# Performance work log

Measured on AMD Instinct MI355X. Metric: run time of the kernel, lower is better.

## Reference

```python
import jax, jax.numpy as jnp
import numpy as np

TEMPERATURE = 0.5  # module buffer `temperature`


def setup_inputs() -> dict:
    key = jax.random.key(0)
    emb_in = jax.random.normal(key, (8192, 1024), dtype=jnp.float32)
    return {"emb_in": emb_in}


def reference(emb_in):
    B = emb_in.shape[0]
    n = B // 4  # loop bound in the original module
    # F.normalize(emb_in, dim=1); after normalization cosine_similarity == dot product
    z = emb_in / jnp.linalg.norm(emb_in, axis=1, keepdims=True)
    S = jnp.matmul(z, z.T) / jnp.float32(TEMPERATURE)  # [B, B] sim / temperature
    rows = S[:n]  # only rows i < n are ever used               # [n, B]
    idx = jnp.arange(n)
    exp_rows = jnp.exp(rows)
    # denominator_i = sum_{k != i} exp(sim[i,k]/T) over the FULL batch dimension
    denom = exp_rows.sum(axis=1) - exp_rows[idx, idx]           # [n]
    log_denom = jnp.log(denom)
    # loss_ij = -(S[i,j] - log(denom_i)); summed over i < j < n.
    # For each i there are (n-1-i) values of j, each contributing log_denom[i].
    counts = (n - 1) - idx                                      # [n]
    sum_sim = jnp.sum(jnp.triu(rows[:, :n], k=1))               # sum_{i<j} S[i,j]/T
    loss = jnp.sum(counts.astype(log_denom.dtype) * log_denom) - sum_sim
    return (-2.0 / n) * (n - 1) * loss
```

## Files before the change

### kernel.cpp

```cpp
#include <hip/hip_runtime.h>
#include <stdint.h>


#define BDIM 1024
#define BROWS 8192
#define NROWS 2048

#define BM 128
#define BN 256
#define BKB 128
#define NKT (BDIM / BKB)

typedef __attribute__((ext_vector_type(4))) int i32x4;
typedef __attribute__((ext_vector_type(8))) int i32x8;
typedef __attribute__((ext_vector_type(4))) float f32x4;

static __device__ __forceinline__ unsigned char f2e4m3(float x) {
  uint32_t u = __float_as_uint(x);
  uint32_t s = (u >> 24) & 0x80u;
  uint32_t a = u & 0x7fffffffu;
  if (a == 0) return (unsigned char)s;
  int e = (int)(a >> 23) - 127;
  uint32_t m = a & 0x7fffffu;
  if (e >= -6) {
    uint32_t keep = m >> 20;
    uint32_t rest = m & 0xfffffu;
    keep += (rest > 0x80000u) || (rest == 0x80000u && (keep & 1u));
    uint32_t v = ((uint32_t)(e + 7) << 3) + keep;
    return (unsigned char)(s | v);
  }
  if (e < -10) return (unsigned char)s;
  uint32_t full = 0x800000u | m;
  int sh = 14 - e;
  uint32_t keep = full >> sh;
  uint32_t rest = full & ((1u << sh) - 1u);
  uint32_t half = 1u << (sh - 1);
  keep += (rest > half) || (rest == half && (keep & 1u));
  return (unsigned char)(s | keep);
}

static __device__ __forceinline__ void gload_lds16(const unsigned char* g, unsigned char* l) {
  __builtin_amdgcn_global_load_lds(
      (const __attribute__((address_space(1))) uint32_t*)(const void*)g,
      (__attribute__((address_space(3))) uint32_t*)(void*)l,
      16, 0, 0);
}

static __device__ __forceinline__ uint32_t pk4(float4 v, float inv) {
  return (uint32_t)f2e4m3(v.x * inv) | ((uint32_t)f2e4m3(v.y * inv) << 8) |
         ((uint32_t)f2e4m3(v.z * inv) << 16) | ((uint32_t)f2e4m3(v.w * inv) << 24);
}

__global__ __launch_bounds__(256) void normalize_kernel(const float* __restrict__ emb,
                                                        unsigned char* __restrict__ zb,
                                                        float* __restrict__ denom,
                                                        float* __restrict__ sumsim) {
  const int w = threadIdx.x >> 6;
  const int lane = threadIdx.x & 63;
  const int row = blockIdx.x * 4 + w;
  const float4* src = reinterpret_cast<const float4*>(emb + (size_t)row * BDIM);
  float4 v[4];
  float ss = 0.f;
#pragma unroll
  for (int i = 0; i < 4; i++) {
    v[i] = src[lane * 4 + i];
    ss += v[i].x * v[i].x + v[i].y * v[i].y + v[i].z * v[i].z + v[i].w * v[i].w;
  }
#pragma unroll
  for (int m = 1; m < 64; m <<= 1) ss += __shfl_xor(ss, m);
  const float inv = rsqrtf(ss);
  uint4 o;
  o.x = pk4(v[0], inv);
  o.y = pk4(v[1], inv);
  o.z = pk4(v[2], inv);
  o.w = pk4(v[3], inv);
  const int cp = (lane & 56) | ((lane & 7) ^ (row & 7));
  *reinterpret_cast<uint4*>(zb + (size_t)row * BDIM + cp * 16) = o;
  if (blockIdx.x < NROWS / 4 && lane == 0) denom[row] = 0.f;
  if (blockIdx.x == 0 && threadIdx.x == 0) sumsim[0] = 0.f;
}


__global__ __launch_bounds__(512, 4) void gemm_fused(const unsigned char* __restrict__ zb,
                                                     float* __restrict__ denom,
                                                     float* __restrict__ sumsim) {
  __shared__ unsigned char As[BM * BKB];
  __shared__ unsigned char Bs[BN * BKB];

  const int bx = blockIdx.x;
  const int xcd = bx & 7;
  const int idx = bx >> 3;
  const int jb = xcd * 4 + (idx & 3);
  const int ib = idx >> 2;
  const int i0 = ib * BM;
  const int j0 = jb * BN;

  const int t = threadIdx.x;
  const int lane = t & 63;
  const int w = t >> 6;
  const int WR = w >> 2;
  const int WC = w & 3;

  const int rsh = lane >> 3;
  const int lin = (lane & 7) * 16;

  const int q2 = lane >> 4;
  const int rsub = lane & 15;
  const int rk = rsub & 7;

  f32x4 acc[4][4] = {};

#define STG_A(g, kk) \
  gload_lds16(zb + (size_t)(i0 + (g) * 8 + rsh) * BDIM + (kk) + lin, &As[(g) * 8 * BKB])
#define STG_B(g, kk) \
  gload_lds16(zb + (size_t)(j0 + (g) * 8 + rsh) * BDIM + (kk) + lin, &Bs[(g) * 8 * BKB])

#define RD_FRAG(dst, base, row)                                                                                  \
  {                                                                                                              \
    const i32x4 lo = *reinterpret_cast<const i32x4*>(&base[(size_t)(row) * BKB + (((2 * q2) ^ rk) * 16)]);       \
    const i32x4 hi = *reinterpret_cast<const i32x4*>(&base[(size_t)(row) * BKB + (((2 * q2 + 1) ^ rk) * 16)]);   \
    dst[0] = lo[0]; dst[1] = lo[1]; dst[2] = lo[2]; dst[3] = lo[3];                                              \
    dst[4] = hi[0]; dst[5] = hi[1]; dst[6] = hi[2]; dst[7] = hi[3];                                              \
  }

#pragma unroll 1
  for (int kt = 0; kt < NKT; ++kt) {
    const int kk = kt * BKB;
    STG_A(2 * w, kk); STG_A(2 * w + 1, kk);
    STG_B(4 * w, kk); STG_B(4 * w + 1, kk);
    STG_B(4 * w + 2, kk); STG_B(4 * w + 3, kk);
    __syncthreads();

    i32x8 bb[4];
#pragma unroll
    for (int nn = 0; nn < 4; nn++) {
      RD_FRAG(bb[nn], Bs, WC * 64 + nn * 16 + rsub);
    }
    __builtin_amdgcn_s_setprio(1);
#pragma unroll
    for (int mm = 0; mm < 4; mm++) {
      i32x8 aa;
      RD_FRAG(aa, As, WR * 64 + mm * 16 + rsub);
#pragma unroll
      for (int nn = 0; nn < 4; nn++) {
        acc[mm][nn] = __builtin_amdgcn_mfma_scale_f32_16x16x128_f8f6f4(
            aa, bb[nn], acc[mm][nn], 0, 0, 0, 0x7f7f7f7f, 0, 0x7f7f7f7f);
      }
    }
    __builtin_amdgcn_s_setprio(0);
    __syncthreads();
  }

  const int hi4 = lane >> 4;
  const int col_l = lane & 15;
  float ssim = 0.f;
#pragma unroll
  for (int m = 0; m < 4; m++) {
    const int gibase = i0 + WR * 64 + m * 16 + hi4 * 4;
#pragma unroll
    for (int r = 0; r < 4; r++) {
      const int gi = gibase + r;
      float dsum = 0.f;
#pragma unroll
      for (int n = 0; n < 4; n++) {
        const int gj = j0 + WC * 64 + n * 16 + col_l;
        const float s = acc[m][n][r] * 2.0f;
        const float e = __expf(s);
        if (gj != gi) dsum += e;
        if (gj < NROWS && gi < gj) ssim += s;
      }
      dsum += __shfl_xor(dsum, 1);
      dsum += __shfl_xor(dsum, 2);
      dsum += __shfl_xor(dsum, 4);
      dsum += __shfl_xor(dsum, 8);
      if (col_l == 0) atomicAdd(&denom[gi], dsum);
    }
  }
#pragma unroll
  for (int msk = 1; msk < 64; msk <<= 1) ssim += __shfl_xor(ssim, msk);
  if (lane == 0 && j0 < NROWS) atomicAdd(sumsim, ssim);
}

__global__ __launch_bounds__(1024) void finalize(const float* __restrict__ denom,
                                                 const float* __restrict__ sumsim,
                                                 float* __restrict__ out) {
  const int t = threadIdx.x;
  double s = 0.0;
#pragma unroll
  for (int i = t; i < NROWS; i += 1024) {
    s += (double)(NROWS - 1 - i) * log((double)denom[i]);
  }
#pragma unroll
  for (int m = 1; m < 64; m <<= 1) s += __shfl_xor(s, m);
  __shared__ double ws_[16];
  if ((t & 63) == 0) ws_[t >> 6] = s;
  __syncthreads();
  if (t == 0) {
    double tot = 0.0;
#pragma unroll
    for (int i = 0; i < 16; i++) tot += ws_[i];
    const double loss = tot - (double)sumsim[0];
    out[0] = (float)(-2.0 / (double)NROWS * (double)(NROWS - 1) * loss);
  }
}

extern "C" void kernel_launch(void* const* d_in, const int* in_sizes, int n_in,
                              void* d_out, int out_size, void* d_ws, size_t ws_size,
                              hipStream_t stream) {
  const float* emb = (const float*)d_in[0];
  unsigned char* zb = (unsigned char*)d_ws;
  float* denom = (float*)((char*)d_ws + (size_t)BROWS * BDIM);
  float* sumsim = denom + NROWS;
  float* out = (float*)d_out;

  normalize_kernel<<<BROWS / 4, 256, 0, stream>>>(emb, zb, denom, sumsim);
  gemm_fused<<<(NROWS / BM) * (BROWS / BN), 512, 0, stream>>>(zb, denom, sumsim);
  finalize<<<1, 1024, 0, stream>>>(denom, sumsim, out);
}
```

Baseline: 59.02 us.

## Prefetch next K tile into registers while computing current tile

Replaces direct global-to-LDS loads with register-staged loads. The next K tile is issued before the MFMA loop and written to LDS after a barrier, so global latency overlaps with compute. This adds six uint4 registers per thread, which puts pressure on the 4-waves occupancy bound, and adds an extra barrier per iteration because LDS is still single-buffered.

```diff
diff --git a/kernel.cpp b/kernel.cpp
--- a/kernel.cpp
+++ b/kernel.cpp
@@ -39,13 +39,6 @@
   return (unsigned char)(s | keep);
 }
 
-static __device__ __forceinline__ void gload_lds16(const unsigned char* g, unsigned char* l) {
-  __builtin_amdgcn_global_load_lds(
-      (const __attribute__((address_space(1))) uint32_t*)(const void*)g,
-      (__attribute__((address_space(3))) uint32_t*)(void*)l,
-      16, 0, 0);
-}
-
 static __device__ __forceinline__ uint32_t pk4(float4 v, float inv) {
   return (uint32_t)f2e4m3(v.x * inv) | ((uint32_t)f2e4m3(v.y * inv) << 8) |
          ((uint32_t)f2e4m3(v.z * inv) << 16) | ((uint32_t)f2e4m3(v.w * inv) << 24);
@@ -103,17 +96,37 @@
 
   const int rsh = lane >> 3;
   const int lin = (lane & 7) * 16;
+  const unsigned char* gA0 = zb + (size_t)(i0 + (2 * w) * 8 + rsh) * BDIM + lin;
+  const unsigned char* gA1 = zb + (size_t)(i0 + (2 * w + 1) * 8 + rsh) * BDIM + lin;
+  const unsigned char* gB0 = zb + (size_t)(j0 + (4 * w) * 8 + rsh) * BDIM + lin;
+  const unsigned char* gB1 = zb + (size_t)(j0 + (4 * w + 1) * 8 + rsh) * BDIM + lin;
+  const unsigned char* gB2 = zb + (size_t)(j0 + (4 * w + 2) * 8 + rsh) * BDIM + lin;
+  const unsigned char* gB3 = zb + (size_t)(j0 + (4 * w + 3) * 8 + rsh) * BDIM + lin;
+  uint4* lA0 = reinterpret_cast<uint4*>(&As[((2 * w) * 8 + rsh) * BKB + lin]);
+  uint4* lA1 = reinterpret_cast<uint4*>(&As[((2 * w + 1) * 8 + rsh) * BKB + lin]);
+  uint4* lB0 = reinterpret_cast<uint4*>(&Bs[((4 * w) * 8 + rsh) * BKB + lin]);
+  uint4* lB1 = reinterpret_cast<uint4*>(&Bs[((4 * w + 1) * 8 + rsh) * BKB + lin]);
+  uint4* lB2 = reinterpret_cast<uint4*>(&Bs[((4 * w + 2) * 8 + rsh) * BKB + lin]);
+  uint4* lB3 = reinterpret_cast<uint4*>(&Bs[((4 * w + 3) * 8 + rsh) * BKB + lin]);
 
   const int q2 = lane >> 4;
   const int rsub = lane & 15;
   const int rk = rsub & 7;
 
   f32x4 acc[4][4] = {};
-
-#define STG_A(g, kk) \
-  gload_lds16(zb + (size_t)(i0 + (g) * 8 + rsh) * BDIM + (kk) + lin, &As[(g) * 8 * BKB])
-#define STG_B(g, kk) \
-  gload_lds16(zb + (size_t)(j0 + (g) * 8 + rsh) * BDIM + (kk) + lin, &Bs[(g) * 8 * BKB])
+  uint4 pA0, pA1, pB0, pB1, pB2, pB3;
+
+#define LOADP(kk)                                                       \
+  {                                                                     \
+    pA0 = *reinterpret_cast<const uint4*>(gA0 + (kk));                  \
+    pA1 = *reinterpret_cast<const uint4*>(gA1 + (kk));                  \
+    pB0 = *reinterpret_cast<const uint4*>(gB0 + (kk));                  \
+    pB1 = *reinterpret_cast<const uint4*>(gB1 + (kk));                  \
+    pB2 = *reinterpret_cast<const uint4*>(gB2 + (kk));                  \
+    pB3 = *reinterpret_cast<const uint4*>(gB3 + (kk));                  \
+  }
+#define WRITEP()                                                        \
+  { *lA0 = pA0; *lA1 = pA1; *lB0 = pB0; *lB1 = pB1; *lB2 = pB2; *lB3 = pB3; }
 
 #define RD_FRAG(dst, base, row)                                                                                  \
   {                                                                                                              \
@@ -123,13 +136,13 @@
     dst[4] = hi[0]; dst[5] = hi[1]; dst[6] = hi[2]; dst[7] = hi[3];                                              \
   }
 
+  LOADP(0);
+  WRITEP();
+  __syncthreads();
+
 #pragma unroll 1
   for (int kt = 0; kt < NKT; ++kt) {
-    const int kk = kt * BKB;
-    STG_A(2 * w, kk); STG_A(2 * w + 1, kk);
-    STG_B(4 * w, kk); STG_B(4 * w + 1, kk);
-    STG_B(4 * w + 2, kk); STG_B(4 * w + 3, kk);
-    __syncthreads();
+    if (kt + 1 < NKT) LOADP((kt + 1) * BKB);
 
     i32x8 bb[4];
 #pragma unroll
@@ -148,7 +161,12 @@
       }
     }
     __builtin_amdgcn_s_setprio(0);
+
     __syncthreads();
+    if (kt + 1 < NKT) {
+      WRITEP();
+      __syncthreads();
+    }
   }
 
   const int hi4 = lane >> 4;
```

Result: slower. 177.3 us (+200.5%).

## Pre-tile FP8 embeddings into MFMA fragment-order units for contiguous loads

Applied to the files above, without the earlier changes.

The normalize kernel now writes the FP8 matrix in 16-row by 128-byte units, with bytes already arranged so each lane's MFMA fragment sits at lane*16 and lane*16+1024. The GEMM stages each unit with two fully contiguous 1KB global-to-LDS loads and reads fragments with plain linear LDS accesses, dropping the XOR swizzle arithmetic. The intent is better coalescing of global loads and conflict-free LDS reads. It ties the workspace layout to the tile shape.

```diff
diff --git a/kernel.cpp b/kernel.cpp
--- a/kernel.cpp
+++ b/kernel.cpp
@@ -8,8 +8,7 @@
 
 #define BM 128
 #define BN 256
-#define BKB 128
-#define NKT (BDIM / BKB)
+#define NKT 8
 
 typedef __attribute__((ext_vector_type(4))) int i32x4;
 typedef __attribute__((ext_vector_type(8))) int i32x8;
@@ -74,8 +73,9 @@
   o.y = pk4(v[1], inv);
   o.z = pk4(v[2], inv);
   o.w = pk4(v[3], inv);
-  const int cp = (lane & 56) | ((lane & 7) ^ (row & 7));
-  *reinterpret_cast<uint4*>(zb + (size_t)row * BDIM + cp * 16) = o;
+  const size_t unit = (size_t)(row >> 4) * 8 + (lane >> 3);
+  const int off = (lane & 1) * 1024 + ((((lane >> 1) & 3) * 16 + (row & 15)) * 16);
+  *reinterpret_cast<uint4*>(zb + unit * 2048 + off) = o;
   if (blockIdx.x < NROWS / 4 && lane == 0) denom[row] = 0.f;
   if (blockIdx.x == 0 && threadIdx.x == 0) sumsim[0] = 0.f;
 }
@@ -84,8 +84,8 @@
 __global__ __launch_bounds__(512, 4) void gemm_fused(const unsigned char* __restrict__ zb,
                                                      float* __restrict__ denom,
                                                      float* __restrict__ sumsim) {
-  __shared__ unsigned char As[BM * BKB];
-  __shared__ unsigned char Bs[BN * BKB];
+  __shared__ unsigned char As[8 * 2048];
+  __shared__ unsigned char Bs[16 * 2048];
 
   const int bx = blockIdx.x;
   const int xcd = bx & 7;
@@ -94,6 +94,8 @@
   const int ib = idx >> 2;
   const int i0 = ib * BM;
   const int j0 = jb * BN;
+  const int i16 = i0 >> 4;
+  const int j16 = j0 >> 4;
 
   const int t = threadIdx.x;
   const int lane = t & 63;
@@ -101,46 +103,45 @@
   const int WR = w >> 2;
   const int WC = w & 3;
 
-  const int rsh = lane >> 3;
-  const int lin = (lane & 7) * 16;
-
-  const int q2 = lane >> 4;
-  const int rsub = lane & 15;
-  const int rk = rsub & 7;
-
   f32x4 acc[4][4] = {};
 
-#define STG_A(g, kk) \
-  gload_lds16(zb + (size_t)(i0 + (g) * 8 + rsh) * BDIM + (kk) + lin, &As[(g) * 8 * BKB])
-#define STG_B(g, kk) \
-  gload_lds16(zb + (size_t)(j0 + (g) * 8 + rsh) * BDIM + (kk) + lin, &Bs[(g) * 8 * BKB])
-
-#define RD_FRAG(dst, base, row)                                                                                  \
-  {                                                                                                              \
-    const i32x4 lo = *reinterpret_cast<const i32x4*>(&base[(size_t)(row) * BKB + (((2 * q2) ^ rk) * 16)]);       \
-    const i32x4 hi = *reinterpret_cast<const i32x4*>(&base[(size_t)(row) * BKB + (((2 * q2 + 1) ^ rk) * 16)]);   \
-    dst[0] = lo[0]; dst[1] = lo[1]; dst[2] = lo[2]; dst[3] = lo[3];                                              \
-    dst[4] = hi[0]; dst[5] = hi[1]; dst[6] = hi[2]; dst[7] = hi[3];                                              \
+#define RDU(dst, base, u)                                                   \
+  {                                                                         \
+    const unsigned char* p_ = (base) + (u) * 2048 + lane * 16;              \
+    const i32x4 lo_ = *reinterpret_cast<const i32x4*>(p_);                  \
+    const i32x4 hi_ = *reinterpret_cast<const i32x4*>(p_ + 1024);           \
+    dst[0] = lo_[0]; dst[1] = lo_[1]; dst[2] = lo_[2]; dst[3] = lo_[3];     \
+    dst[4] = hi_[0]; dst[5] = hi_[1]; dst[6] = hi_[2]; dst[7] = hi_[3];     \
   }
 
 #pragma unroll 1
   for (int kt = 0; kt < NKT; ++kt) {
-    const int kk = kt * BKB;
-    STG_A(2 * w, kk); STG_A(2 * w + 1, kk);
-    STG_B(4 * w, kk); STG_B(4 * w + 1, kk);
-    STG_B(4 * w + 2, kk); STG_B(4 * w + 3, kk);
+    {
+      const unsigned char* sa = zb + (((size_t)(i16 + w)) * 8 + kt) * 2048 + lane * 16;
+      unsigned char* da = As + w * 2048;
+      gload_lds16(sa, da);
+      gload_lds16(sa + 1024, da + 1024);
+#pragma unroll
+      for (int uu = 0; uu < 2; ++uu) {
+        const int u = 2 * w + uu;
+        const unsigned char* sb = zb + (((size_t)(j16 + u)) * 8 + kt) * 2048 + lane * 16;
+        unsigned char* db = Bs + u * 2048;
+        gload_lds16(sb, db);
+        gload_lds16(sb + 1024, db + 1024);
+      }
+    }
     __syncthreads();
 
     i32x8 bb[4];
 #pragma unroll
     for (int nn = 0; nn < 4; nn++) {
-      RD_FRAG(bb[nn], Bs, WC * 64 + nn * 16 + rsub);
+      RDU(bb[nn], Bs, WC * 4 + nn);
     }
     __builtin_amdgcn_s_setprio(1);
 #pragma unroll
     for (int mm = 0; mm < 4; mm++) {
       i32x8 aa;
-      RD_FRAG(aa, As, WR * 64 + mm * 16 + rsub);
+      RDU(aa, As, WR * 4 + mm);
 #pragma unroll
       for (int nn = 0; nn < 4; nn++) {
         acc[mm][nn] = __builtin_amdgcn_mfma_scale_f32_16x16x128_f8f6f4(
```

Result: faster. 57.00 us (-3.4%).
